# Kernel optimization log

Measured on AMD Instinct MI355X. Metric: run time of the kernel, lower is better.

The kernel has to match this reference:

```python
import jax, jax.numpy as jnp
import numpy as np

B, N, D = 1, 1024, 3584
H, KVH, HD = 28, 4, 128
I = 18944
SEC = [16, 24, 24]  # mrope_section, sums to HD//2
EPS_RMS = 1e-6
EPS_SM = 1e-6


def setup_inputs() -> dict:
    key = jax.random.key(0)
    ks = jax.random.split(key, 16)
    s = 0.02
    return {
        "hidden_states": jax.random.normal(ks[0], (B, N, D), jnp.float32),
        "cos": jax.random.uniform(ks[1], (3, B, N, HD), jnp.float32, -1.0, 1.0),
        "sin": jax.random.uniform(ks[2], (3, B, N, HD), jnp.float32, -1.0, 1.0),
        "prune_mask": jax.random.randint(ks[3], (B, N), 0, 2, jnp.int32),
        "Wq": jax.random.normal(ks[4], (D, H * HD), jnp.float32) * s,
        "bq": jnp.zeros((H * HD,), jnp.float32),
        "Wk": jax.random.normal(ks[5], (D, KVH * HD), jnp.float32) * s,
        "bk": jnp.zeros((KVH * HD,), jnp.float32),
        "Wv": jax.random.normal(ks[6], (D, KVH * HD), jnp.float32) * s,
        "bv": jnp.zeros((KVH * HD,), jnp.float32),
        "Wo": jax.random.normal(ks[7], (H * HD, D), jnp.float32) * s,
        "ln1_w": jnp.ones((D,), jnp.float32),
        "ln2_w": jnp.ones((D,), jnp.float32),
        "Wg": jax.random.normal(ks[8], (D, I), jnp.float32) * s,
        "Wu": jax.random.normal(ks[9], (D, I), jnp.float32) * s,
        "Wd": jax.random.normal(ks[10], (I, D), jnp.float32) * s,
    }


def _rmsnorm(x, w):
    v = jnp.mean(x * x, axis=-1, keepdims=True)
    return x * jax.lax.rsqrt(v + EPS_RMS) * w


def _rotate_half(x):
    h = x.shape[-1] // 2
    return jnp.concatenate([-x[..., h:], x[..., :h]], axis=-1)


def _mrope_select(t):
    # t: (3, B, N, HD) -> (B, 1, N, HD), picking section i from axis i%3
    parts, idx = [], 0
    for i, s in enumerate(SEC * 2):
        parts.append(t[i % 3, :, :, idx:idx + s])
        idx += s
    return jnp.concatenate(parts, axis=-1)[:, None]


def reference(hidden_states, cos, sin, prune_mask, Wq, bq, Wk, bk, Wv, bv, Wo,
              ln1_w, ln2_w, Wg, Wu, Wd):
    x = _rmsnorm(hidden_states, ln1_w)
    q = (x @ Wq + bq).reshape(B, N, H, HD).transpose(0, 2, 1, 3)
    k = (x @ Wk + bk).reshape(B, N, KVH, HD).transpose(0, 2, 1, 3)
    v = (x @ Wv + bv).reshape(B, N, KVH, HD).transpose(0, 2, 1, 3)

    cf, sf = _mrope_select(cos), _mrope_select(sin)
    q = q * cf + _rotate_half(q) * sf
    k = k * cf + _rotate_half(k) * sf

    groups = H // KVH
    k = jnp.repeat(k, groups, axis=1)  # (B,H,N,HD)
    v = jnp.repeat(v, groups, axis=1)

    scores = jnp.einsum("bhqd,bhkd->bhqk", q, k) / np.sqrt(HD).astype(np.float32)
    causal = jnp.tril(jnp.ones((N, N), bool))
    scores = jnp.where(causal, scores, jnp.float32(-1e9))

    # custom prune-masked softmax (softmax_with_mask)
    am = prune_mask.astype(jnp.float32)[:, None, None, :]  # (B,1,1,N)
    eye = jnp.eye(N, dtype=jnp.float32)
    am = am + (1.0 - am) * eye
    mx = jnp.max(scores, axis=-1, keepdims=True)
    e = jnp.exp(scores - mx) * am
    attn = (e + EPS_SM / N) / (jnp.sum(e, axis=-1, keepdims=True) + EPS_SM)

    o = jnp.einsum("bhqk,bhkd->bhqd", attn, v)
    o = o.transpose(0, 2, 1, 3).reshape(B, N, H * HD) @ Wo

    h = hidden_states + o
    y = _rmsnorm(h, ln2_w)
    mlp = (jax.nn.silu(y @ Wg) * (y @ Wu)) @ Wd
    return h + mlp
```

## Files before the change

### kernel.cpp

```cpp
#include <hip/hip_runtime.h>
#include <hip/hip_bf16.h>


#define SEQ   1024
#define DIM   3584
#define NH    28
#define NKVH  4
#define HDIM  128
#define IDIM  18944
#define QKVN  4608
#define GUN   37888

typedef __attribute__((ext_vector_type(8))) __bf16 bf16x8;
typedef __attribute__((ext_vector_type(4))) __bf16 bf16x4;
typedef __attribute__((ext_vector_type(4))) float  f32x4;

static constexpr size_t OFF_WQKVT = 0;
static constexpr size_t OFF_WOT   = OFF_WQKVT + (size_t)QKVN*DIM*2;
static constexpr size_t OFF_WGUT  = OFF_WOT   + (size_t)DIM*DIM*2;
static constexpr size_t OFF_WDT   = OFF_WGUT  + (size_t)GUN*DIM*2;
static constexpr size_t OFF_XB    = OFF_WDT   + (size_t)DIM*IDIM*2;
static constexpr size_t OFF_QKV   = OFF_XB    + (size_t)SEQ*DIM*2;
static constexpr size_t OFF_VT    = OFF_QKV   + (size_t)SEQ*QKVN*2;
static constexpr size_t OFF_VSUMP = OFF_VT    + (size_t)NKVH*HDIM*SEQ*2;
static constexpr size_t OFF_VSUM  = OFF_VSUMP + 4*8*128*4;
static constexpr size_t OFF_BQKV  = OFF_VSUM  + 4*128*4;
static constexpr size_t OFF_OB    = OFF_BQKV  + (size_t)QKVN*4;
static constexpr size_t OFF_HB    = OFF_OB    + (size_t)SEQ*DIM*2;
static constexpr size_t OFF_YB    = OFF_HB    + (size_t)SEQ*DIM*4;
static constexpr size_t OFF_GU    = OFF_YB    + (size_t)SEQ*DIM*2;
static constexpr size_t OFF_PB    = OFF_GU    + (size_t)SEQ*GUN*2;
static constexpr size_t OFF_PART  = OFF_GU;

#define GLL16(gp, lp)                                                        \
  __builtin_amdgcn_global_load_lds(                                         \
      (const __attribute__((address_space(1))) void*)(gp),                  \
      (__attribute__((address_space(3))) void*)(lp), 16, 0, 0)

#define BAR    asm volatile("s_barrier" ::: "memory")
#define SCHEDB __builtin_amdgcn_sched_barrier(0)

__global__ __launch_bounds__(256) void transconv_kernel(
    const float* __restrict__ W, __bf16* __restrict__ WT, int K, int N)
{
  __shared__ __bf16 t[64][72];
  const int tid = threadIdx.x;
  const int k0 = blockIdx.y * 64, n0 = blockIdx.x * 64;
#pragma unroll
  for (int it = 0; it < 4; ++it) {
    int idx = it * 256 + tid;
    int r = idx >> 4, c4 = idx & 15;
    float4 v = *(const float4*)(W + (size_t)(k0 + r) * N + n0 + c4 * 4);
    t[r][c4 * 4 + 0] = (__bf16)v.x;
    t[r][c4 * 4 + 1] = (__bf16)v.y;
    t[r][c4 * 4 + 2] = (__bf16)v.z;
    t[r][c4 * 4 + 3] = (__bf16)v.w;
  }
  __syncthreads();
#pragma unroll
  for (int it = 0; it < 2; ++it) {
    int idx = it * 256 + tid;
    int r = idx >> 3, c8 = idx & 7;
    bf16x8 o;
#pragma unroll
    for (int i = 0; i < 8; ++i) o[i] = t[c8 * 8 + i][r];
    *(bf16x8*)(WT + (size_t)(n0 + r) * K + k0 + c8 * 8) = o;
  }
}

__global__ __launch_bounds__(256) void pack_bias_kernel(
    const float* __restrict__ bq, const float* __restrict__ bk,
    const float* __restrict__ bv, float* __restrict__ out)
{
  int i = blockIdx.x * 256 + threadIdx.x;
  if (i < DIM) out[i] = bq[i];
  else if (i < DIM + 512) out[i] = bk[i - DIM];
  else if (i < QKVN) out[i] = bv[i - DIM - 512];
}

__global__ __launch_bounds__(256) void rmsnorm_kernel(
    const float* __restrict__ in, const float* __restrict__ w,
    __bf16* __restrict__ out)
{
  const int row = blockIdx.x;
  const int t = threadIdx.x;
  const float* x = in + (size_t)row * DIM;
  float4 v[4];
  float ss = 0.f;
#pragma unroll
  for (int i = 0; i < 4; ++i) {
    int idx = t + i * 256;
    if (idx < 896) {
      v[i] = ((const float4*)x)[idx];
      ss += v[i].x * v[i].x + v[i].y * v[i].y + v[i].z * v[i].z + v[i].w * v[i].w;
    }
  }
#pragma unroll
  for (int m = 1; m < 64; m <<= 1) ss += __shfl_xor(ss, m);
  __shared__ float red[4];
  if ((t & 63) == 0) red[t >> 6] = ss;
  __syncthreads();
  float tot = red[0] + red[1] + red[2] + red[3];
  float rs = rsqrtf(tot / (float)DIM + 1e-6f);
#pragma unroll
  for (int i = 0; i < 4; ++i) {
    int idx = t + i * 256;
    if (idx < 896) {
      float4 wv = ((const float4*)w)[idx];
      bf16x4 o;
      o[0] = (__bf16)(v[i].x * rs * wv.x);
      o[1] = (__bf16)(v[i].y * rs * wv.y);
      o[2] = (__bf16)(v[i].z * rs * wv.z);
      o[3] = (__bf16)(v[i].w * rs * wv.w);
      *(bf16x4*)(out + (size_t)row * DIM + idx * 4) = o;
    }
  }
}

__global__ __launch_bounds__(256, 2) void gemm_splitk_kernel(
    const __bf16* __restrict__ A, const __bf16* __restrict__ BT,
    float* __restrict__ PART, int M, int N, int K, int Kc, int gridY)
{
  __shared__ __bf16 As[128 * 64];
  __shared__ __bf16 Bs[128 * 64];
  const int tid = threadIdx.x;
  const int l = tid & 63, w = tid >> 6;

  const int nwg = gridDim.x;
  const int bq8 = nwg >> 3, br8 = nwg & 7;
  const int xcd = blockIdx.x & 7, bidx = blockIdx.x >> 3;
  const int wg = (xcd < br8 ? xcd * (bq8 + 1) : br8 * (bq8 + 1) + (xcd - br8) * bq8) + bidx;
  const int tm = wg % gridY;
  const int wg2 = wg / gridY;
  const int gridX = N >> 7;
  const int tn = wg2 % gridX;
  const int ks = wg2 / gridX;
  const int row0 = tm * 128;
  const int col0 = tn * 128;
  const int kbase = ks * Kc;

  const int m0 = (w >> 1) * 64;
  const int n0 = (w & 1) * 64;
  const int lg = l >> 4, lc = l & 15;

  f32x4 acc[4][4] = {};

  size_t aoff[4], boff[4];
  int lbyte[4];
#pragma unroll
  for (int it = 0; it < 4; ++it) {
    const int cbase = (it * 4 + w) * 64;
    const int c = cbase + l;
    const int r = c >> 3, p = c & 7;
    const int b = p ^ (r & 7);
    aoff[it] = (size_t)(row0 + r) * K + kbase + b * 8;
    boff[it] = (size_t)(col0 + r) * K + kbase + b * 8;
    lbyte[it] = cbase * 16;
  }
  const int sw = lc & 7;

  const int ktc = Kc >> 6;
  for (int kt = 0; kt < ktc; ++kt) {
    const int k0 = kt << 6;
#pragma unroll
    for (int it = 0; it < 4; ++it) {
      GLL16(A + aoff[it] + k0, (char*)As + lbyte[it]);
      GLL16(BT + boff[it] + k0, (char*)Bs + lbyte[it]);
    }
    __syncthreads();
#pragma unroll
    for (int s = 0; s < 2; ++s) {
      bf16x8 af[4], bfv[4];
#pragma unroll
      for (int a = 0; a < 4; ++a)
        af[a] = *(const bf16x8*)(As + (m0 + a * 16 + lc) * 64 + ((s * 4 + lg) ^ sw) * 8);
#pragma unroll
      for (int b = 0; b < 4; ++b)
        bfv[b] = *(const bf16x8*)(Bs + (n0 + b * 16 + lc) * 64 + ((s * 4 + lg) ^ sw) * 8);
#pragma unroll
      for (int a = 0; a < 4; ++a)
#pragma unroll
        for (int b = 0; b < 4; ++b)
          acc[a][b] = __builtin_amdgcn_mfma_f32_16x16x32_bf16(af[a], bfv[b], acc[a][b], 0, 0, 0);
    }
    __syncthreads();
  }

  float* P = PART + (size_t)ks * M * N;
  const int lr = lg * 4;
#pragma unroll
  for (int b = 0; b < 4; ++b) {
    const int col = col0 + n0 + b * 16 + lc;
#pragma unroll
    for (int a = 0; a < 4; ++a)
#pragma unroll
      for (int j = 0; j < 4; ++j)
        P[(size_t)(row0 + m0 + a * 16 + lr + j) * N + col] = acc[a][b][j];
  }
}

template<int S, bool BF16OUT, bool BIAS>
__global__ __launch_bounds__(256) void reduce_kernel(
    const float* __restrict__ part, const float* __restrict__ resid,
    const float* __restrict__ bias, void* __restrict__ out, int N, int MN4)
{
  const int i4 = blockIdx.x * 256 + threadIdx.x;
  if (i4 >= MN4) return;
  const size_t base = (size_t)i4 * 4;
  f32x4 s = *(const f32x4*)(part + base);
#pragma unroll
  for (int k = 1; k < S; ++k)
    s += *(const f32x4*)(part + (size_t)k * MN4 * 4 + base);
  if (BIAS) {
    const int col = (int)(base % N);
    s += *(const f32x4*)(bias + col);
  }
  if (resid != nullptr) s += *(const f32x4*)(resid + base);
  if (BF16OUT) {
    bf16x4 o;
#pragma unroll
    for (int j = 0; j < 4; ++j) o[j] = (__bf16)s[j];
    *(bf16x4*)((__bf16*)out + base) = o;
  } else {
    *(f32x4*)((float*)out + base) = s;
  }
}

__global__ __launch_bounds__(512, 1) void gemm256_kernel(
    const __bf16* __restrict__ A, const __bf16* __restrict__ BT,
    __bf16* __restrict__ C, int M, int N, int K, int gridY)
{
  __shared__ int4 lds4[8192];
  char* ldsc = (char*)lds4;
  const int tid = threadIdx.x;
  const int l = tid & 63, w = tid >> 6;
  const int wr = w >> 2, wc = w & 3;
  const int lg = l >> 4, lc = l & 15;

  const int nwg = gridDim.x;
  const int bq8 = nwg >> 3, br8 = nwg & 7;
  const int xcd = blockIdx.x & 7, bidx = blockIdx.x >> 3;
  const int wg = (xcd < br8 ? xcd * (bq8 + 1) : br8 * (bq8 + 1) + (xcd - br8) * bq8) + bidx;
  const int row0 = (wg % gridY) * 256;
  const int col0 = (wg / gridY) * 256;

  size_t aoffj[2], boffj[2];
  int dstj[2];
#pragma unroll
  for (int j = 0; j < 2; ++j) {
    const int c = (j * 8 + w) * 64 + l;
    const int r = c >> 3, p = c & 7;
    const int b = p ^ (r & 7);
    aoffj[j] = (size_t)(row0 + r) * K + b * 8;
    boffj[j] = (size_t)(col0 + r) * K + b * 8;
    dstj[j] = (j * 8 + w) * 1024;
  }

#define STG_A(U, KT, BUFB) do {                                              \
    GLL16(A + aoffj[0] + (size_t)(U) * 128 * K + (size_t)(KT) * 64,          \
          ldsc + (BUFB) + (U) * 16384 + dstj[0]);                            \
    GLL16(A + aoffj[1] + (size_t)(U) * 128 * K + (size_t)(KT) * 64,          \
          ldsc + (BUFB) + (U) * 16384 + dstj[1]); } while (0)
#define STG_B(U, KT, BUFB) do {                                              \
    GLL16(BT + boffj[0] + (size_t)(U) * 128 * K + (size_t)(KT) * 64,         \
          ldsc + (BUFB) + 32768 + (U) * 16384 + dstj[0]);                    \
    GLL16(BT + boffj[1] + (size_t)(U) * 128 * K + (size_t)(KT) * 64,         \
          ldsc + (BUFB) + 32768 + (U) * 16384 + dstj[1]); } while (0)

  const int sw = lc & 7;
  const int rdA = (wr * 128 + lc) * 128;
  const int rdB = 32768 + (wc * 64 + lc) * 128;
  const int sk0 = (lg ^ sw) * 16;
  const int sk1 = ((4 | lg) ^ sw) * 16;

  f32x4 acc[8][4] = {};
  bf16x8 af[4][2], bfr[4][2];

#define RD_A4(MH, BUFB) do { _Pragma("unroll")                               \
    for (int mm = 0; mm < 4; ++mm) {                                         \
      af[mm][0] = *(const bf16x8*)(ldsc + (BUFB) + rdA + ((MH) * 4 + mm) * 2048 + sk0); \
      af[mm][1] = *(const bf16x8*)(ldsc + (BUFB) + rdA + ((MH) * 4 + mm) * 2048 + sk1); } } while (0)
#define RD_B2(NL, BUFB) do { _Pragma("unroll")                               \
    for (int nn = 0; nn < 2; ++nn) {                                         \
      bfr[(NL) + nn][0] = *(const bf16x8*)(ldsc + (BUFB) + rdB + ((NL) + nn) * 2048 + sk0); \
      bfr[(NL) + nn][1] = *(const bf16x8*)(ldsc + (BUFB) + rdB + ((NL) + nn) * 2048 + sk1); } } while (0)

#define MFMA16(MH, NL) do { _Pragma("unroll")                                \
    for (int mm = 0; mm < 4; ++mm) { _Pragma("unroll")                       \
      for (int nn = 0; nn < 2; ++nn) {                                       \
        acc[(MH)*4+mm][(NL)+nn] = __builtin_amdgcn_mfma_f32_16x16x32_bf16(   \
            af[mm][0], bfr[(NL)+nn][0], acc[(MH)*4+mm][(NL)+nn], 0, 0, 0);   \
        acc[(MH)*4+mm][(NL)+nn] = __builtin_amdgcn_mfma_f32_16x16x32_bf16(   \
            af[mm][1], bfr[(NL)+nn][1], acc[(MH)*4+mm][(NL)+nn], 0, 0, 0); } } } while (0)

#define PH_MFMA(MH, NL)                                                      \
    BAR; SCHEDB; __builtin_amdgcn_s_setprio(1);                              \
    MFMA16(MH, NL);                                                          \
    __builtin_amdgcn_s_setprio(0); SCHEDB; BAR

  STG_A(0, 0, 0); STG_A(1, 0, 0); STG_B(0, 0, 0); STG_B(1, 0, 0);
  STG_A(0, 1, 65536); STG_A(1, 1, 65536); STG_B(0, 1, 65536); STG_B(1, 1, 65536);
  asm volatile("s_waitcnt vmcnt(8)" ::: "memory");
  BAR;

  const int T = K >> 6;
#pragma unroll 1
  for (int i = 0; i < (T >> 1); ++i) {
    const int t0 = 2 * i;
    const int se = (t0 + 2 < T) ? t0 + 2 : 0;
    const int so = (t0 + 3 < T) ? t0 + 3 : 0;
    RD_A4(0, 0); RD_B2(0, 0);
    PH_MFMA(0, 0);
    RD_B2(2, 0);
    PH_MFMA(0, 2);
    RD_A4(1, 0);
    PH_MFMA(1, 2);
    STG_A(0, se, 0); STG_A(1, se, 0);
    asm volatile("s_waitcnt vmcnt(4)" ::: "memory");
    PH_MFMA(1, 0);
    RD_A4(0, 65536); RD_B2(0, 65536);
    STG_B(0, se, 0); STG_B(1, se, 0);
    PH_MFMA(0, 0);
    RD_B2(2, 65536);
    PH_MFMA(0, 2);
    RD_A4(1, 65536);
    PH_MFMA(1, 2);
    STG_A(0, so, 65536); STG_A(1, so, 65536);
    STG_B(0, so, 65536); STG_B(1, so, 65536);
    asm volatile("s_waitcnt vmcnt(8)" ::: "memory");
    PH_MFMA(1, 0);
  }
  asm volatile("s_waitcnt vmcnt(0)" ::: "memory");

#pragma unroll
  for (int m = 0; m < 8; ++m)
#pragma unroll
    for (int n = 0; n < 4; ++n)
#pragma unroll
      for (int j = 0; j < 4; ++j)
        C[(size_t)(row0 + wr * 128 + m * 16 + lg * 4 + j) * N
          + (col0 + wc * 64 + n * 16 + lc)] = (__bf16)acc[m][n][j];
#undef STG_A
#undef STG_B
#undef RD_A4
#undef RD_B2
#undef MFMA16
#undef PH_MFMA
}

__global__ __launch_bounds__(256) void rope_kernel(
    __bf16* __restrict__ qkv, const float* __restrict__ cosb,
    const float* __restrict__ sinb)
{
  const int n = blockIdx.x;
  for (int p = threadIdx.x; p < 32 * 64; p += 256) {
    const int head = p >> 6;
    const int d = p & 63;
    const int src = (d < 16) ? 0 : (d < 40) ? 1 : 2;
    const float* cb = cosb + (size_t)src * SEQ * HDIM + (size_t)n * HDIM;
    const float* sb = sinb + (size_t)src * SEQ * HDIM + (size_t)n * HDIM;
    const float c0 = cb[d], c1 = cb[d + 64];
    const float s0 = sb[d], s1 = sb[d + 64];
    const int col = (head < NH) ? head * HDIM : DIM + (head - NH) * HDIM;
    __bf16* q = qkv + (size_t)n * QKVN + col;
    const float a = (float)q[d];
    const float b = (float)q[d + 64];
    q[d]      = (__bf16)(a * c0 - b * s0);
    q[d + 64] = (__bf16)(b * c1 + a * s1);
  }
}

__global__ __launch_bounds__(256) void vtrans_kernel(
    const __bf16* __restrict__ qkv, __bf16* __restrict__ vT,
    float* __restrict__ vsump)
{
  __shared__ __bf16 t[128][132];
  const int nt = blockIdx.x, kvh = blockIdx.y;
  const int n0 = nt * 128;
  const int tid = threadIdx.x;
#pragma unroll
  for (int it = 0; it < 8; ++it) {
    int idx = it * 256 + tid;
    int nl = idx >> 4, c8 = idx & 15;
    bf16x8 v = *(const bf16x8*)(qkv + (size_t)(n0 + nl) * QKVN + 4096 + kvh * HDIM + c8 * 8);
#pragma unroll
    for (int i = 0; i < 8; ++i) t[nl][c8 * 8 + i] = v[i];
  }
  __syncthreads();
#pragma unroll
  for (int it = 0; it < 8; ++it) {
    int idx = it * 256 + tid;
    int d = idx >> 4, c8 = idx & 15;
    bf16x8 o;
#pragma unroll
    for (int i = 0; i < 8; ++i) o[i] = t[c8 * 8 + i][d];
    *(bf16x8*)(vT + (size_t)(kvh * HDIM + d) * SEQ + n0 + c8 * 8) = o;
  }
  if (tid < 128) {
    float s = 0.f;
    for (int nl = 0; nl < 128; ++nl) s += (float)t[nl][tid];
    vsump[(size_t)(kvh * 8 + nt) * 128 + tid] = s;
  }
}

__global__ __launch_bounds__(512) void vsum_reduce_kernel(
    const float* __restrict__ vsump, float* __restrict__ vsum)
{
  const int idx = threadIdx.x;
  const int kvh = idx >> 7, d = idx & 127;
  float s = 0.f;
#pragma unroll
  for (int nt = 0; nt < 8; ++nt) s += vsump[(size_t)(kvh * 8 + nt) * 128 + d];
  vsum[idx] = s;
}

__global__ __launch_bounds__(256) void attn_kernel(
    const __bf16* __restrict__ qkv, const __bf16* __restrict__ vT,
    const float* __restrict__ vsum, const int* __restrict__ prune,
    __bf16* __restrict__ o)
{
  __shared__ __bf16 plds[4 * 16 * 40];
  const int tid = threadIdx.x;
  const int l = tid & 63, w = tid >> 6;
  const int h = blockIdx.y;
  const int kvh = h / 7;
  const int qt = blockIdx.x;
  const int qbase = qt * 64 + w * 16;
  const int lg = l >> 4, lc = l & 15;
  __bf16* pw = plds + w * (16 * 40);

  bf16x8 qf[4];
#pragma unroll
  for (int s = 0; s < 4; ++s)
    qf[s] = *(const bf16x8*)(qkv + (size_t)(qbase + lc) * QKVN + h * HDIM + s * 32 + lg * 8);

  f32x4 oacc[8] = {};
  float mrun[4] = {-3e38f, -3e38f, -3e38f, -3e38f};
  float lrun[4] = {0.f, 0.f, 0.f, 0.f};

  const int kbEnd = ((qbase + 15) >> 5) + 1;
  for (int kb = 0; kb < kbEnd; ++kb) {
    f32x4 sacc[2] = {};
#pragma unroll
    for (int s = 0; s < 4; ++s) {
#pragma unroll
      for (int c = 0; c < 2; ++c) {
        bf16x8 kf = *(const bf16x8*)(qkv + (size_t)(kb * 32 + c * 16 + lc) * QKVN
                                     + DIM + kvh * HDIM + s * 32 + lg * 8);
        sacc[c] = __builtin_amdgcn_mfma_f32_16x16x32_bf16(qf[s], kf, sacc[c], 0, 0, 0);
      }
    }
    float p[2][4];
    int am[2];
#pragma unroll
    for (int c = 0; c < 2; ++c) {
      const int col = kb * 32 + c * 16 + lc;
      am[c] = (prune[col] != 0) ? 1 : 0;
#pragma unroll
      for (int j = 0; j < 4; ++j) {
        const int row = qbase + lg * 4 + j;
        float sv = sacc[c][j] * 0.08838834764831845f;
        p[c][j] = (col <= row) ? sv : -3e38f;
      }
    }
#pragma unroll
    for (int j = 0; j < 4; ++j) {
      float mx = fmaxf(p[0][j], p[1][j]);
      mx = fmaxf(mx, __shfl_xor(mx, 1));
      mx = fmaxf(mx, __shfl_xor(mx, 2));
      mx = fmaxf(mx, __shfl_xor(mx, 4));
      mx = fmaxf(mx, __shfl_xor(mx, 8));
      const float mnew = fmaxf(mrun[j], mx);
      const float scale = __expf(mrun[j] - mnew);
      mrun[j] = mnew;
      const int row = qbase + lg * 4 + j;
      float rs = 0.f;
#pragma unroll
      for (int c = 0; c < 2; ++c) {
        const int col = kb * 32 + c * 16 + lc;
        float e = __expf(p[c][j] - mnew);
        const int keep = (col == row) ? 1 : am[c];
        e = keep ? e : 0.f;
        p[c][j] = e;
        rs += e;
      }
      rs += __shfl_xor(rs, 1);
      rs += __shfl_xor(rs, 2);
      rs += __shfl_xor(rs, 4);
      rs += __shfl_xor(rs, 8);
      lrun[j] = lrun[j] * scale + rs;
#pragma unroll
      for (int df = 0; df < 8; ++df) oacc[df][j] *= scale;
    }
#pragma unroll
    for (int c = 0; c < 2; ++c)
#pragma unroll
      for (int j = 0; j < 4; ++j)
        pw[(lg * 4 + j) * 40 + c * 16 + lc] = (__bf16)p[c][j];
    bf16x8 pa = *(const bf16x8*)(pw + lc * 40 + lg * 8);
#pragma unroll
    for (int df = 0; df < 8; ++df) {
      bf16x8 vf = *(const bf16x8*)(vT + (size_t)(kvh * HDIM + df * 16 + lc) * SEQ + kb * 32 + lg * 8);
      oacc[df] = __builtin_amdgcn_mfma_f32_16x16x32_bf16(pa, vf, oacc[df], 0, 0, 0);
    }
  }
#pragma unroll
  for (int df = 0; df < 8; ++df) {
    const float vs = vsum[kvh * HDIM + df * 16 + lc];
#pragma unroll
    for (int j = 0; j < 4; ++j) {
      const int row = qbase + lg * 4 + j;
      const float denom = lrun[j] + 1e-6f;
      const float val = (oacc[df][j] + 9.765625e-10f * vs) / denom;
      o[(size_t)row * DIM + h * HDIM + df * 16 + lc] = (__bf16)val;
    }
  }
}

__global__ __launch_bounds__(256) void silu_mul_kernel(
    const __bf16* __restrict__ gu, __bf16* __restrict__ p)
{
  const int n = blockIdx.y;
  const int i8 = blockIdx.x * 256 + threadIdx.x;
  if (i8 >= IDIM / 8) return;
  bf16x8 g = *(const bf16x8*)(gu + (size_t)n * GUN + i8 * 8);
  bf16x8 u = *(const bf16x8*)(gu + (size_t)n * GUN + IDIM + i8 * 8);
  bf16x8 o;
#pragma unroll
  for (int i = 0; i < 8; ++i) {
    const float gf = (float)g[i];
    const float uf = (float)u[i];
    const float s = gf / (1.f + __expf(-gf));
    o[i] = (__bf16)(s * uf);
  }
  *(bf16x8*)(p + (size_t)n * IDIM + i8 * 8) = o;
}

extern "C" void kernel_launch(void* const* d_in, const int* in_sizes, int n_in,
                              void* d_out, int out_size, void* d_ws, size_t ws_size,
                              hipStream_t stream) {
  const float* hidden = (const float*)d_in[0];
  const float* cosb   = (const float*)d_in[1];
  const float* sinb   = (const float*)d_in[2];
  const int*   prune  = (const int*)d_in[3];
  const float* Wq     = (const float*)d_in[4];
  const float* bq     = (const float*)d_in[5];
  const float* Wk     = (const float*)d_in[6];
  const float* bk     = (const float*)d_in[7];
  const float* Wv     = (const float*)d_in[8];
  const float* bv     = (const float*)d_in[9];
  const float* Wo     = (const float*)d_in[10];
  const float* ln1    = (const float*)d_in[11];
  const float* ln2    = (const float*)d_in[12];
  const float* Wg     = (const float*)d_in[13];
  const float* Wu     = (const float*)d_in[14];
  const float* Wd     = (const float*)d_in[15];
  float* out = (float*)d_out;
  char* ws = (char*)d_ws;

  __bf16* WQKVT = (__bf16*)(ws + OFF_WQKVT);
  __bf16* WOT   = (__bf16*)(ws + OFF_WOT);
  __bf16* WGUT  = (__bf16*)(ws + OFF_WGUT);
  __bf16* WDT   = (__bf16*)(ws + OFF_WDT);
  __bf16* XB    = (__bf16*)(ws + OFF_XB);
  __bf16* QKV   = (__bf16*)(ws + OFF_QKV);
  __bf16* VT    = (__bf16*)(ws + OFF_VT);
  float*  VSUMP = (float*)(ws + OFF_VSUMP);
  float*  VSUM  = (float*)(ws + OFF_VSUM);
  float*  BQKV  = (float*)(ws + OFF_BQKV);
  __bf16* OB    = (__bf16*)(ws + OFF_OB);
  float*  HB    = (float*)(ws + OFF_HB);
  __bf16* YB    = (__bf16*)(ws + OFF_YB);
  __bf16* GU    = (__bf16*)(ws + OFF_GU);
  __bf16* PB    = (__bf16*)(ws + OFF_PB);
  float*  PART  = (float*)(ws + OFF_PART);

  transconv_kernel<<<dim3(DIM / 64, DIM / 64), 256, 0, stream>>>(Wq, WQKVT, DIM, DIM);
  transconv_kernel<<<dim3(512 / 64, DIM / 64), 256, 0, stream>>>(Wk, WQKVT + (size_t)DIM * DIM, DIM, 512);
  transconv_kernel<<<dim3(512 / 64, DIM / 64), 256, 0, stream>>>(Wv, WQKVT + (size_t)4096 * DIM, DIM, 512);
  transconv_kernel<<<dim3(DIM / 64, DIM / 64), 256, 0, stream>>>(Wo, WOT, DIM, DIM);
  transconv_kernel<<<dim3(IDIM / 64, DIM / 64), 256, 0, stream>>>(Wg, WGUT, DIM, IDIM);
  transconv_kernel<<<dim3(IDIM / 64, DIM / 64), 256, 0, stream>>>(Wu, WGUT + (size_t)IDIM * DIM, DIM, IDIM);
  transconv_kernel<<<dim3(DIM / 64, IDIM / 64), 256, 0, stream>>>(Wd, WDT, IDIM, DIM);

  pack_bias_kernel<<<QKVN / 256, 256, 0, stream>>>(bq, bk, bv, BQKV);

  rmsnorm_kernel<<<SEQ, 256, 0, stream>>>(hidden, ln1, XB);

  gemm_splitk_kernel<<<(QKVN / 128) * (SEQ / 128) * 2, 256, 0, stream>>>(
      XB, WQKVT, PART, SEQ, QKVN, DIM, DIM / 2, SEQ / 128);
  reduce_kernel<2, true, true><<<(SEQ * QKVN / 4 + 255) / 256, 256, 0, stream>>>(
      PART, nullptr, BQKV, QKV, QKVN, SEQ * QKVN / 4);

  rope_kernel<<<SEQ, 256, 0, stream>>>(QKV, cosb, sinb);

  vtrans_kernel<<<dim3(8, NKVH), 256, 0, stream>>>(QKV, VT, VSUMP);
  vsum_reduce_kernel<<<1, 512, 0, stream>>>(VSUMP, VSUM);

  attn_kernel<<<dim3(SEQ / 64, NH), 256, 0, stream>>>(QKV, VT, VSUM, prune, OB);

  gemm_splitk_kernel<<<(DIM / 128) * (SEQ / 128) * 2, 256, 0, stream>>>(
      OB, WOT, PART, SEQ, DIM, DIM, DIM / 2, SEQ / 128);
  reduce_kernel<2, false, false><<<(SEQ * DIM / 4 + 255) / 256, 256, 0, stream>>>(
      PART, hidden, nullptr, HB, DIM, SEQ * DIM / 4);

  rmsnorm_kernel<<<SEQ, 256, 0, stream>>>(HB, ln2, YB);

  gemm256_kernel<<<(GUN / 256) * (SEQ / 256), 512, 0, stream>>>(
      YB, WGUT, GU, SEQ, GUN, DIM, SEQ / 256);

  silu_mul_kernel<<<dim3(10, SEQ), 256, 0, stream>>>(GU, PB);

  gemm_splitk_kernel<<<(DIM / 128) * (SEQ / 128) * 4, 256, 0, stream>>>(
      PB, WDT, PART, SEQ, DIM, IDIM, IDIM / 4, SEQ / 128);
  reduce_kernel<4, false, false><<<(SEQ * DIM / 4 + 255) / 256, 256, 0, stream>>>(
      PART, HB, nullptr, out, DIM, SEQ * DIM / 4);
}
```

Baseline: 1.049 ms.

## Fuse SiLU-mul into gate/up GEMM epilogue and use 256-tile split-K GEMM

```diff
diff --git a/kernel.cpp b/kernel.cpp
--- a/kernel.cpp
+++ b/kernel.cpp
@@ -41,7 +41,7 @@
 #define SCHEDB __builtin_amdgcn_sched_barrier(0)
 
 __global__ __launch_bounds__(256) void transconv_kernel(
-    const float* __restrict__ W, __bf16* __restrict__ WT, int K, int N)
+    const float* __restrict__ W, __bf16* __restrict__ WT, int K, int N, int mode)
 {
   __shared__ __bf16 t[64][72];
   const int tid = threadIdx.x;
@@ -64,7 +64,10 @@
     bf16x8 o;
 #pragma unroll
     for (int i = 0; i < 8; ++i) o[i] = t[c8 * 8 + i][r];
-    *(bf16x8*)(WT + (size_t)(n0 + r) * K + k0 + c8 * 8) = o;
+    const int nlog = n0 + r;
+    const int orow = (mode == 0) ? nlog
+                   : ((nlog >> 4) << 5) + ((mode == 2) ? 16 : 0) + (nlog & 15);
+    *(bf16x8*)(WT + (size_t)orow * K + k0 + c8 * 8) = o;
   }
 }
 
@@ -226,9 +229,10 @@
   }
 }
 
+template<int EPI>
 __global__ __launch_bounds__(512, 1) void gemm256_kernel(
     const __bf16* __restrict__ A, const __bf16* __restrict__ BT,
-    __bf16* __restrict__ C, int M, int N, int K, int gridY)
+    void* __restrict__ OUT, int M, int N, int K, int Kc, int gridY)
 {
   __shared__ int4 lds4[8192];
   char* ldsc = (char*)lds4;
@@ -241,8 +245,12 @@
   const int bq8 = nwg >> 3, br8 = nwg & 7;
   const int xcd = blockIdx.x & 7, bidx = blockIdx.x >> 3;
   const int wg = (xcd < br8 ? xcd * (bq8 + 1) : br8 * (bq8 + 1) + (xcd - br8) * bq8) + bidx;
+  const int ntn = N >> 8;
+  const int wg2 = wg / gridY;
   const int row0 = (wg % gridY) * 256;
-  const int col0 = (wg / gridY) * 256;
+  const int col0 = (wg2 % ntn) * 256;
+  const int ks = wg2 / ntn;
+  const int kbase = ks * Kc;
 
   size_t aoffj[2], boffj[2];
   int dstj[2];
@@ -251,8 +259,8 @@
     const int c = (j * 8 + w) * 64 + l;
     const int r = c >> 3, p = c & 7;
     const int b = p ^ (r & 7);
-    aoffj[j] = (size_t)(row0 + r) * K + b * 8;
-    boffj[j] = (size_t)(col0 + r) * K + b * 8;
+    aoffj[j] = (size_t)(row0 + r) * K + kbase + b * 8;
+    boffj[j] = (size_t)(col0 + r) * K + kbase + b * 8;
     dstj[j] = (j * 8 + w) * 1024;
   }
 
@@ -303,7 +311,7 @@
   asm volatile("s_waitcnt vmcnt(8)" ::: "memory");
   BAR;
 
-  const int T = K >> 6;
+  const int T = Kc >> 6;
 #pragma unroll 1
   for (int i = 0; i < (T >> 1); ++i) {
     const int t0 = 2 * i;
@@ -332,14 +340,36 @@
   }
   asm volatile("s_waitcnt vmcnt(0)" ::: "memory");
 
-#pragma unroll
-  for (int m = 0; m < 8; ++m)
-#pragma unroll
-    for (int n = 0; n < 4; ++n)
-#pragma unroll
-      for (int j = 0; j < 4; ++j)
-        C[(size_t)(row0 + wr * 128 + m * 16 + lg * 4 + j) * N
-          + (col0 + wc * 64 + n * 16 + lc)] = (__bf16)acc[m][n][j];
+  if (EPI == 0) {
+    __bf16* PBo = (__bf16*)OUT;
+    const int id = N >> 1;
+    const int baseq = (col0 + wc * 64) >> 5;
+#pragma unroll
+    for (int m = 0; m < 8; ++m) {
+#pragma unroll
+      for (int p = 0; p < 2; ++p) {
+        const int gcol = (baseq + p) * 16 + lc;
+#pragma unroll
+        for (int j = 0; j < 4; ++j) {
+          const int row = row0 + wr * 128 + m * 16 + lg * 4 + j;
+          const float g = acc[m][2 * p][j];
+          const float u = acc[m][2 * p + 1][j];
+          const float s = g / (1.f + __expf(-g));
+          PBo[(size_t)row * id + gcol] = (__bf16)(s * u);
+        }
+      }
+    }
+  } else {
+    float* P = (float*)OUT + (size_t)ks * M * N;
+#pragma unroll
+    for (int m = 0; m < 8; ++m)
+#pragma unroll
+      for (int n = 0; n < 4; ++n)
+#pragma unroll
+        for (int j = 0; j < 4; ++j)
+          P[(size_t)(row0 + wr * 128 + m * 16 + lg * 4 + j) * N
+            + (col0 + wc * 64 + n * 16 + lc)] = acc[m][n][j];
+  }
 #undef STG_A
 #undef STG_B
 #undef RD_A4
@@ -515,25 +545,6 @@
       o[(size_t)row * DIM + h * HDIM + df * 16 + lc] = (__bf16)val;
     }
   }
-}
-
-__global__ __launch_bounds__(256) void silu_mul_kernel(
-    const __bf16* __restrict__ gu, __bf16* __restrict__ p)
-{
-  const int n = blockIdx.y;
-  const int i8 = blockIdx.x * 256 + threadIdx.x;
-  if (i8 >= IDIM / 8) return;
-  bf16x8 g = *(const bf16x8*)(gu + (size_t)n * GUN + i8 * 8);
-  bf16x8 u = *(const bf16x8*)(gu + (size_t)n * GUN + IDIM + i8 * 8);
-  bf16x8 o;
-#pragma unroll
-  for (int i = 0; i < 8; ++i) {
-    const float gf = (float)g[i];
-    const float uf = (float)u[i];
-    const float s = gf / (1.f + __expf(-gf));
-    o[i] = (__bf16)(s * uf);
-  }
-  *(bf16x8*)(p + (size_t)n * IDIM + i8 * 8) = o;
 }
 
 extern "C" void kernel_launch(void* const* d_in, const int* in_sizes, int n_in,
@@ -571,20 +582,13 @@
   __bf16* OB    = (__bf16*)(ws + OFF_OB);
   float*  HB    = (float*)(ws + OFF_HB);
   __bf16* YB    = (__bf16*)(ws + OFF_YB);
-  __bf16* GU    = (__bf16*)(ws + OFF_GU);
   __bf16* PB    = (__bf16*)(ws + OFF_PB);
   float*  PART  = (float*)(ws + OFF_PART);
 
-  transconv_kernel<<<dim3(DIM / 64, DIM / 64), 256, 0, stream>>>(Wq, WQKVT, DIM, DIM);
-  transconv_kernel<<<dim3(512 / 64, DIM / 64), 256, 0, stream>>>(Wk, WQKVT + (size_t)DIM * DIM, DIM, 512);
-  transconv_kernel<<<dim3(512 / 64, DIM / 64), 256, 0, stream>>>(Wv, WQKVT + (size_t)4096 * DIM, DIM, 512);
-  transconv_kernel<<<dim3(DIM / 64, DIM / 64), 256, 0, stream>>>(Wo, WOT, DIM, DIM);
-  transconv_kernel<<<dim3(IDIM / 64, DIM / 64), 256, 0, stream>>>(Wg, WGUT, DIM, IDIM);
-  transconv_kernel<<<dim3(IDIM / 64, DIM / 64), 256, 0, stream>>>(Wu, WGUT + (size_t)IDIM * DIM, DIM, IDIM);
-  transconv_kernel<<<dim3(DIM / 64, IDIM / 64), 256, 0, stream>>>(Wd, WDT, IDIM, DIM);
-
+  transconv_kernel<<<dim3(DIM / 64, DIM / 64), 256, 0, stream>>>(Wq, WQKVT, DIM, DIM, 0);
+  transconv_kernel<<<dim3(512 / 64, DIM / 64), 256, 0, stream>>>(Wk, WQKVT + (size_t)DIM * DIM, DIM, 512, 0);
+  transconv_kernel<<<dim3(512 / 64, DIM / 64), 256, 0, stream>>>(Wv, WQKVT + (size_t)4096 * DIM, DIM, 512, 0);
   pack_bias_kernel<<<QKVN / 256, 256, 0, stream>>>(bq, bk, bv, BQKV);
-
   rmsnorm_kernel<<<SEQ, 256, 0, stream>>>(hidden, ln1, XB);
 
   gemm_splitk_kernel<<<(QKVN / 128) * (SEQ / 128) * 2, 256, 0, stream>>>(
@@ -593,26 +597,26 @@
       PART, nullptr, BQKV, QKV, QKVN, SEQ * QKVN / 4);
 
   rope_kernel<<<SEQ, 256, 0, stream>>>(QKV, cosb, sinb);
-
   vtrans_kernel<<<dim3(8, NKVH), 256, 0, stream>>>(QKV, VT, VSUMP);
   vsum_reduce_kernel<<<1, 512, 0, stream>>>(VSUMP, VSUM);
-
   attn_kernel<<<dim3(SEQ / 64, NH), 256, 0, stream>>>(QKV, VT, VSUM, prune, OB);
 
-  gemm_splitk_kernel<<<(DIM / 128) * (SEQ / 128) * 2, 256, 0, stream>>>(
-      OB, WOT, PART, SEQ, DIM, DIM, DIM / 2, SEQ / 128);
-  reduce_kernel<2, false, false><<<(SEQ * DIM / 4 + 255) / 256, 256, 0, stream>>>(
+  transconv_kernel<<<dim3(DIM / 64, DIM / 64), 256, 0, stream>>>(Wo, WOT, DIM, DIM, 0);
+  gemm256_kernel<1><<<(DIM / 256) * (SEQ / 256) * 4, 512, 0, stream>>>(
+      OB, WOT, PART, SEQ, DIM, DIM, DIM / 4, SEQ / 256);
+  reduce_kernel<4, false, false><<<(SEQ * DIM / 4 + 255) / 256, 256, 0, stream>>>(
       PART, hidden, nullptr, HB, DIM, SEQ * DIM / 4);
 
   rmsnorm_kernel<<<SEQ, 256, 0, stream>>>(HB, ln2, YB);
 
-  gemm256_kernel<<<(GUN / 256) * (SEQ / 256), 512, 0, stream>>>(
-      YB, WGUT, GU, SEQ, GUN, DIM, SEQ / 256);
-
-  silu_mul_kernel<<<dim3(10, SEQ), 256, 0, stream>>>(GU, PB);
-
-  gemm_splitk_kernel<<<(DIM / 128) * (SEQ / 128) * 4, 256, 0, stream>>>(
-      PB, WDT, PART, SEQ, DIM, IDIM, IDIM / 4, SEQ / 128);
+  transconv_kernel<<<dim3(IDIM / 64, DIM / 64), 256, 0, stream>>>(Wg, WGUT, DIM, IDIM, 1);
+  transconv_kernel<<<dim3(IDIM / 64, DIM / 64), 256, 0, stream>>>(Wu, WGUT, DIM, IDIM, 2);
+  gemm256_kernel<0><<<(GUN / 256) * (SEQ / 256), 512, 0, stream>>>(
+      YB, WGUT, PB, SEQ, GUN, DIM, DIM, SEQ / 256);
+
+  transconv_kernel<<<dim3(DIM / 64, IDIM / 64), 256, 0, stream>>>(Wd, WDT, IDIM, DIM, 0);
+  gemm256_kernel<1><<<(DIM / 256) * (SEQ / 256) * 4, 512, 0, stream>>>(
+      PB, WDT, PART, SEQ, DIM, IDIM, IDIM / 4, SEQ / 256);
   reduce_kernel<4, false, false><<<(SEQ * DIM / 4 + 255) / 256, 256, 0, stream>>>(
       PART, HB, nullptr, out, DIM, SEQ * DIM / 4);
 }
```

Result: faster. 986.6 us (-6.0%).
